# Optimization experiments

Measured on AMD Instinct MI355X. Metric: run time of the kernel, lower is better.

The kernel has to match this reference:

```python
import jax, jax.numpy as jnp
import numpy as np
from jax import lax

# ViT-B/16 geometry hard-coded by the source (197 tokens, 12 heads, head rep of 12)
B, C, IMG, PATCH = 32, 3, 224, 16
E, H, L, P = 768, 12, 12, 16          # embed dim, heads, layers, VPT prompts per layer
NP = (IMG // PATCH) ** 2 + 1          # 197 = cls + 196 patches
S = NP + P                            # 213 tokens after prompt append
HD = E // H
FF = 4 * E
EPS = 1e-6
SCALE = 1.0 / float(HD) ** 0.5


def setup_inputs() -> dict:
    key = jax.random.key(0)
    ks = jax.random.split(key, 12)
    s = 0.02
    return {
        "x": jax.random.normal(ks[0], (B, C, IMG, IMG), jnp.float32),
        "cofficient": jax.random.uniform(ks[1], (L, 1, P), jnp.float32),
        "patch_w": jax.random.normal(ks[2], (E, C, PATCH, PATCH), jnp.float32) * s,
        "patch_b": jnp.zeros((E,), jnp.float32),
        "cls": jax.random.normal(ks[3], (1, 1, E), jnp.float32) * s,
        "pos": jax.random.normal(ks[4], (1, NP, E), jnp.float32) * s,
        "ln_pre_g": jnp.ones((E,), jnp.float32),
        "ln_pre_b": jnp.zeros((E,), jnp.float32),
        "prompts": jax.random.normal(ks[5], (L, P, E), jnp.float32) * s,
        "ln1_g": jnp.ones((L, E), jnp.float32),
        "ln1_b": jnp.zeros((L, E), jnp.float32),
        "qkv_w": jax.random.normal(ks[6], (L, 3 * E, E), jnp.float32) * s,
        "qkv_b": jnp.zeros((L, 3 * E), jnp.float32),
        "proj_w": jax.random.normal(ks[7], (L, E, E), jnp.float32) * s,
        "proj_b": jnp.zeros((L, E), jnp.float32),
        "ln2_g": jnp.ones((L, E), jnp.float32),
        "ln2_b": jnp.zeros((L, E), jnp.float32),
        "fc1_w": jax.random.normal(ks[8], (L, FF, E), jnp.float32) * s,
        "fc1_b": jnp.zeros((L, FF), jnp.float32),
        "fc2_w": jax.random.normal(ks[9], (L, E, FF), jnp.float32) * s,
        "fc2_b": jnp.zeros((L, E), jnp.float32),
        "ln_post_g": jnp.ones((E,), jnp.float32),
        "ln_post_b": jnp.zeros((E,), jnp.float32),
    }


def _ln(x, g, b):
    m = jnp.mean(x, -1, keepdims=True)
    v = jnp.mean(jnp.square(x - m), -1, keepdims=True)
    return (x - m) * lax.rsqrt(v + EPS) * g + b


def reference(x, cofficient, patch_w, patch_b, cls, pos, ln_pre_g, ln_pre_b,
              prompts, ln1_g, ln1_b, qkv_w, qkv_b, proj_w, proj_b,
              ln2_g, ln2_b, fc1_w, fc1_b, fc2_w, fc2_b, ln_post_g, ln_post_b):
    # patch embedding: conv16/16 -> [B, E, 14, 14] -> [B, 196, E]
    h = lax.conv_general_dilated(x, patch_w, (PATCH, PATCH), 'VALID',
                                 dimension_numbers=('NCHW', 'OIHW', 'NCHW'))
    h = h + patch_b[None, :, None, None]
    h = h.reshape(B, E, NP - 1).transpose(0, 2, 1)
    h = jnp.concatenate([jnp.broadcast_to(cls, (B, 1, E)), h], axis=1) + pos
    h = _ln(h, ln_pre_g, ln_pre_b)
    # pad to fixed seq length S; prompt slots are overwritten inside each block
    h = jnp.concatenate([h, jnp.zeros((B, P, E), h.dtype)], axis=1)

    def block(xc, p):
        prompt, coeff, g1, b1, wqkv, bqkv, wo, bo, g2, b2, w1, bb1, w2, bb2 = p
        # deep VPT: replace prompt tokens each layer
        xc = jnp.concatenate([xc[:, :NP], jnp.broadcast_to(prompt[None], (B, P, E))], axis=1)
        hh = _ln(xc, g1, b1)
        qkv = jnp.einsum('bse,fe->bsf', hh, wqkv) + bqkv
        q, k, v = jnp.split(qkv, 3, axis=-1)
        q = q.reshape(B, S, H, HD).transpose(0, 2, 1, 3)
        k = k.reshape(B, S, H, HD).transpose(0, 2, 1, 3)
        v = v.reshape(B, S, H, HD).transpose(0, 2, 1, 3)
        scores = jnp.einsum('bhqd,bhkd->bhqk', q, k) * SCALE   # [B,H,S,S]
        # elementwise coefficient reweighting: ones over 197 base keys, coeff over prompts
        cfull = jnp.concatenate([jnp.ones((NP,), scores.dtype), coeff[0]])
        scores = scores * cfull[None, None, None, :]
        attn = jax.nn.softmax(scores, axis=-1)
        o = jnp.einsum('bhqk,bhkd->bhqd', attn, v).transpose(0, 2, 1, 3).reshape(B, S, E)
        xc = xc + (jnp.einsum('bse,fe->bsf', o, wo) + bo)
        hh = _ln(xc, g2, b2)
        hh = jax.nn.gelu(jnp.einsum('bse,fe->bsf', hh, w1) + bb1, approximate=False)
        xc = xc + (jnp.einsum('bsf,ef->bse', hh, w2) + bb2)
        return xc, None

    params = (prompts, cofficient, ln1_g, ln1_b, qkv_w, qkv_b, proj_w, proj_b,
              ln2_g, ln2_b, fc1_w, fc1_b, fc2_w, fc2_b)
    h, _ = lax.scan(block, h, params)
    return _ln(h[:, 0, :], ln_post_g, ln_post_b)   # [B, E]
```

## Files before the change

kernel.cpp:

```cpp
#include <hip/hip_runtime.h>
#include <hip/hip_bf16.h>

#define B_   32
#define S_   213
#define NP_  197
#define P_   16
#define E_   768
#define H_   12
#define HD_  64
#define FF_  3072
#define L_   12
#define EPS_ 1e-6f
#define SCALE_ 0.125f

typedef __attribute__((ext_vector_type(8))) short short8;
typedef __attribute__((ext_vector_type(4))) float floatx4;

__device__ __forceinline__ ushort f2b(float x) {
  __hip_bfloat16 h = __float2bfloat16(x);
  return __builtin_bit_cast(ushort, h);
}
__device__ __forceinline__ float b2f(ushort u) {
  return __uint_as_float(((unsigned)u) << 16);
}

__device__ __forceinline__ void glds16(const void* g, void* l) {
  __builtin_amdgcn_global_load_lds(
      (const __attribute__((address_space(1))) void*)g,
      (__attribute__((address_space(3))) void*)l, 16, 0, 0);
}

template <int MODE>
__global__ __launch_bounds__(256) void gemm_mfma(
    const ushort* __restrict__ A, const ushort* __restrict__ W,
    const float* __restrict__ bias, float* __restrict__ Cf,
    ushort* __restrict__ Cb, ushort* __restrict__ Vout,
    int M, int N, int K) {
  __shared__ alignas(16) ushort Al[4096];
  __shared__ alignas(16) ushort Wl[4096];
  const int tid = threadIdx.x;
  const int w = tid >> 6, l = tid & 63;
  const int m0 = blockIdx.y * 128, n0 = blockIdx.x * 128;
  const int rw = (w >> 1) * 64, cw = (w & 1) * 64;

  const int mA0 = min(m0 + l, M - 1);
  const int mA1 = min(m0 + 64 + l, M - 1);
  const ushort* Ag0 = A + (size_t)mA0 * K + w * 8;
  const ushort* Ag1 = A + (size_t)mA1 * K + w * 8;
  const ushort* Wg0 = W + (size_t)(n0 + l) * K + w * 8;
  const ushort* Wg1 = W + (size_t)(n0 + 64 + l) * K + w * 8;
  ushort* Ald0 = &Al[w * 1024];
  ushort* Ald1 = &Al[w * 1024 + 512];
  ushort* Wld0 = &Wl[w * 1024];
  ushort* Wld1 = &Wl[w * 1024 + 512];

  floatx4 acc[4][4];
#pragma unroll
  for (int i = 0; i < 4; ++i)
#pragma unroll
    for (int j = 0; j < 4; ++j) acc[i][j] = (floatx4){0.f, 0.f, 0.f, 0.f};

  const int lm = l & 15, lk = l >> 4;

  for (int k0 = 0; k0 < K; k0 += 32) {
    glds16(Ag0 + k0, Ald0);
    glds16(Ag1 + k0, Ald1);
    glds16(Wg0 + k0, Wld0);
    glds16(Wg1 + k0, Wld1);
    __syncthreads();
    short8 af[4], bf[4];
#pragma unroll
    for (int s = 0; s < 4; ++s) {
      af[s] = *(const short8*)&Al[(size_t)(lk * 128 + rw + s * 16 + lm) * 8];
      bf[s] = *(const short8*)&Wl[(size_t)(lk * 128 + cw + s * 16 + lm) * 8];
    }
#pragma unroll
    for (int i = 0; i < 4; ++i)
#pragma unroll
      for (int j = 0; j < 4; ++j)
        acc[i][j] = __builtin_amdgcn_mfma_f32_16x16x32_bf16(
            af[i], bf[j], acc[i][j], 0, 0, 0);
    __syncthreads();
  }

  const int lq = l >> 4;
#pragma unroll
  for (int i = 0; i < 4; ++i) {
    const int row0 = m0 + rw + i * 16 + lq * 4;
#pragma unroll
    for (int j = 0; j < 4; ++j) {
      const int col = n0 + cw + j * 16 + lm;
      const float bc = bias[col];
#pragma unroll
      for (int r = 0; r < 4; ++r) {
        const int row = row0 + r;
        if (row >= M) continue;
        float v = acc[i][j][r] + bc;
        if (MODE == 0) Cb[(size_t)row * N + col] = f2b(v);
        if (MODE == 1) {
          v = 0.5f * v * (1.0f + erff(v * 0.70710678118654752f));
          Cb[(size_t)row * N + col] = f2b(v);
        }
        if (MODE == 2) Cf[(size_t)row * N + col] += v;
        if (MODE == 3) {
          if (col < 1536) {
            Cb[(size_t)row * 1536 + col] = f2b(v);
          } else {
            const int c = col - 1536, hh = c >> 6, dd = c & 63;
            const int bb = row / 213, ss = row % 213;
            Vout[(((size_t)(bb * 12 + hh) * 28 + (ss >> 3)) * 64 + dd) * 8 +
                 (ss & 7)] = f2b(v);
          }
        }
      }
    }
  }
}

__global__ __launch_bounds__(256) void patch_mfma(
    const ushort* __restrict__ xb, const ushort* __restrict__ pwb,
    const float* __restrict__ pb, const float* __restrict__ pos,
    float* __restrict__ xc) {
  __shared__ alignas(16) ushort Al[4096];
  __shared__ alignas(16) ushort Wl[4096];
  const int tid = threadIdx.x;
  const int w = tid >> 6, l = tid & 63;
  const int m0 = blockIdx.y * 128, n0 = blockIdx.x * 128;
  const int rw = (w >> 1) * 64, cw = (w & 1) * 64;

  const int mA0 = m0 + l, mA1 = m0 + 64 + l;
  const int b0 = mA0 / 196, p0 = mA0 % 196, pr0 = p0 / 14, pc0 = p0 % 14;
  const int b1 = mA1 / 196, p1 = mA1 % 196, pr1 = p1 / 14, pc1 = p1 % 14;
  const ushort* Wg0 = pwb + (size_t)(n0 + l) * 768 + w * 8;
  const ushort* Wg1 = pwb + (size_t)(n0 + 64 + l) * 768 + w * 8;
  ushort* Ald0 = &Al[w * 1024];
  ushort* Ald1 = &Al[w * 1024 + 512];
  ushort* Wld0 = &Wl[w * 1024];
  ushort* Wld1 = &Wl[w * 1024 + 512];

  floatx4 acc[4][4];
#pragma unroll
  for (int i = 0; i < 4; ++i)
#pragma unroll
    for (int j = 0; j < 4; ++j) acc[i][j] = (floatx4){0.f, 0.f, 0.f, 0.f};

  const int lm = l & 15, lk = l >> 4;

  for (int k0 = 0; k0 < 768; k0 += 32) {
    const int k = k0 + w * 8;
    const int c = k >> 8, kh = (k >> 4) & 15, kw = k & 15;
    const ushort* a0 =
        xb + ((size_t)(b0 * 3 + c) * 224 + pr0 * 16 + kh) * 224 + pc0 * 16 + kw;
    const ushort* a1 =
        xb + ((size_t)(b1 * 3 + c) * 224 + pr1 * 16 + kh) * 224 + pc1 * 16 + kw;
    glds16(a0, Ald0);
    glds16(a1, Ald1);
    glds16(Wg0 + k0, Wld0);
    glds16(Wg1 + k0, Wld1);
    __syncthreads();
    short8 af[4], bf[4];
#pragma unroll
    for (int s = 0; s < 4; ++s) {
      af[s] = *(const short8*)&Al[(size_t)(lk * 128 + rw + s * 16 + lm) * 8];
      bf[s] = *(const short8*)&Wl[(size_t)(lk * 128 + cw + s * 16 + lm) * 8];
    }
#pragma unroll
    for (int i = 0; i < 4; ++i)
#pragma unroll
      for (int j = 0; j < 4; ++j)
        acc[i][j] = __builtin_amdgcn_mfma_f32_16x16x32_bf16(
            af[i], bf[j], acc[i][j], 0, 0, 0);
    __syncthreads();
  }

  const int lq = l >> 4;
#pragma unroll
  for (int i = 0; i < 4; ++i) {
    const int row0 = m0 + rw + i * 16 + lq * 4;
#pragma unroll
    for (int j = 0; j < 4; ++j) {
      const int col = n0 + cw + j * 16 + lm;
      const float bc = pb[col];
#pragma unroll
      for (int r = 0; r < 4; ++r) {
        const int row = row0 + r;
        const int bb = row / 196, pp = row % 196, t = pp + 1;
        xc[((size_t)bb * S_ + t) * E_ + col] =
            acc[i][j][r] + bc + pos[(size_t)t * E_ + col];
      }
    }
  }
}

__global__ __launch_bounds__(256) void conv_x_kernel(
    const float* __restrict__ x, const float* __restrict__ pw,
    ushort* __restrict__ xb, ushort* __restrict__ pwb) {
  size_t t = (size_t)blockIdx.x * 256 + threadIdx.x;
  const float4* s;
  ushort* d;
  size_t off;
  if (t < 1204224) { s = (const float4*)x;  d = xb;  off = t; }
  else             { s = (const float4*)pw; d = pwb; off = t - 1204224; }
  float4 v = s[off];
  ushort4 r;
  r.x = f2b(v.x); r.y = f2b(v.y); r.z = f2b(v.z); r.w = f2b(v.w);
  *(ushort4*)(d + off * 4) = r;
}

__global__ __launch_bounds__(256) void conv_w_kernel(
    const float* __restrict__ qkvw, const float* __restrict__ projw,
    const float* __restrict__ f1w, const float* __restrict__ f2w,
    ushort* __restrict__ wq, ushort* __restrict__ wp,
    ushort* __restrict__ w1, ushort* __restrict__ w2) {
  size_t t = (size_t)blockIdx.x * 256 + threadIdx.x;
  const float4* s;
  ushort* d;
  size_t off;
  if (t < 442368)       { s = (const float4*)qkvw; d = wq; off = t; }
  else if (t < 589824)  { s = (const float4*)projw; d = wp; off = t - 442368; }
  else if (t < 1179648) { s = (const float4*)f1w;  d = w1; off = t - 589824; }
  else                  { s = (const float4*)f2w;  d = w2; off = t - 1179648; }
  float4 v = s[off];
  ushort4 r;
  r.x = f2b(v.x); r.y = f2b(v.y); r.z = f2b(v.z); r.w = f2b(v.w);
  *(ushort4*)(d + off * 4) = r;
}

__global__ __launch_bounds__(256) void vt_pad_zero(ushort* __restrict__ vt) {
  int idx = blockIdx.x * 256 + threadIdx.x;
  if (idx >= 384 * 64 * 11) return;
  int bh = idx / 704;
  int rem = idx % 704;
  int d = rem / 11, ee = rem % 11;
  int s = 213 + ee;
  vt[(((size_t)bh * 28 + (s >> 3)) * 64 + d) * 8 + (s & 7)] = 0;
}

__global__ __launch_bounds__(256) void init_cls_prompts(
    const float* __restrict__ cls, const float* __restrict__ pos,
    float* __restrict__ xc) {
  int idx = blockIdx.x;
  int b = idx / 17, s = idx % 17;
  int tid = threadIdx.x;
  if (s == 0) {
    for (int e = tid; e < E_; e += 256)
      xc[(size_t)b * S_ * E_ + e] = cls[e] + pos[e];
  } else {
    int t = 196 + s;
    for (int e = tid; e < E_; e += 256)
      xc[((size_t)b * S_ + t) * E_ + e] = 0.f;
  }
}

__device__ inline float2 block_sums(float s, float q) {
  __shared__ float sm[8];
#pragma unroll
  for (int off = 32; off; off >>= 1) {
    s += __shfl_xor(s, off);
    q += __shfl_xor(q, off);
  }
  int lane = threadIdx.x & 63, wid = threadIdx.x >> 6;
  if (lane == 0) { sm[2 * wid] = s; sm[2 * wid + 1] = q; }
  __syncthreads();
  float2 r;
  r.x = sm[0] + sm[2] + sm[4] + sm[6];
  r.y = sm[1] + sm[3] + sm[5] + sm[7];
  return r;
}

__global__ __launch_bounds__(256) void ln_pre_kernel(
    float* __restrict__ xc, const float* __restrict__ g,
    const float* __restrict__ bb) {
  int idx = blockIdx.x;
  int b = idx / NP_, t = idx % NP_;
  float* row = xc + ((size_t)b * S_ + t) * E_;
  int tid = threadIdx.x;
  float v0 = row[tid], v1 = row[tid + 256], v2 = row[tid + 512];
  float2 r = block_sums(v0 + v1 + v2, v0 * v0 + v1 * v1 + v2 * v2);
  float mean = r.x * (1.f / 768.f);
  float var  = r.y * (1.f / 768.f) - mean * mean;
  float rstd = rsqrtf(var + EPS_);
  row[tid]       = (v0 - mean) * rstd * g[tid]       + bb[tid];
  row[tid + 256] = (v1 - mean) * rstd * g[tid + 256] + bb[tid + 256];
  row[tid + 512] = (v2 - mean) * rstd * g[tid + 512] + bb[tid + 512];
}

__global__ __launch_bounds__(256) void ln_block_kernel(
    float* __restrict__ xc, ushort* __restrict__ hh,
    const float* __restrict__ g, const float* __restrict__ bb,
    const float* __restrict__ prompt) {
  int idx = blockIdx.x;
  int b = idx / S_, t = idx % S_;
  float* row = xc + ((size_t)b * S_ + t) * E_;
  ushort* orow = hh + ((size_t)b * S_ + t) * E_;
  int tid = threadIdx.x;
  float v0, v1, v2;
  if (prompt != nullptr && t >= NP_) {
    const float* pr = prompt + (size_t)(t - NP_) * E_;
    v0 = pr[tid]; v1 = pr[tid + 256]; v2 = pr[tid + 512];
    row[tid] = v0; row[tid + 256] = v1; row[tid + 512] = v2;
  } else {
    v0 = row[tid]; v1 = row[tid + 256]; v2 = row[tid + 512];
  }
  float2 r = block_sums(v0 + v1 + v2, v0 * v0 + v1 * v1 + v2 * v2);
  float mean = r.x * (1.f / 768.f);
  float var  = r.y * (1.f / 768.f) - mean * mean;
  float rstd = rsqrtf(var + EPS_);
  orow[tid]       = f2b((v0 - mean) * rstd * g[tid]       + bb[tid]);
  orow[tid + 256] = f2b((v1 - mean) * rstd * g[tid + 256] + bb[tid + 256]);
  orow[tid + 512] = f2b((v2 - mean) * rstd * g[tid + 512] + bb[tid + 512]);
}

__global__ __launch_bounds__(256) void ln_post_kernel(
    const float* __restrict__ xc, const float* __restrict__ g,
    const float* __restrict__ bb, float* __restrict__ out) {
  int b = blockIdx.x;
  const float* row = xc + (size_t)b * S_ * E_;
  int tid = threadIdx.x;
  float v0 = row[tid], v1 = row[tid + 256], v2 = row[tid + 512];
  float2 r = block_sums(v0 + v1 + v2, v0 * v0 + v1 * v1 + v2 * v2);
  float mean = r.x * (1.f / 768.f);
  float var  = r.y * (1.f / 768.f) - mean * mean;
  float rstd = rsqrtf(var + EPS_);
  out[(size_t)b * E_ + tid]       = (v0 - mean) * rstd * g[tid]       + bb[tid];
  out[(size_t)b * E_ + tid + 256] = (v1 - mean) * rstd * g[tid + 256] + bb[tid + 256];
  out[(size_t)b * E_ + tid + 512] = (v2 - mean) * rstd * g[tid + 512] + bb[tid + 512];
}

__global__ __launch_bounds__(256) void attn_mfma(
    const ushort* __restrict__ qk, const ushort* __restrict__ vt,
    const float* __restrict__ coeff, ushort* __restrict__ o) {
  __shared__ alignas(16) ushort Vts[14336];
  __shared__ alignas(16) ushort Pss[4][3808];
  const int bh = blockIdx.x, h = bh % H_, b = bh / H_;
  const int tid = threadIdx.x, w = tid >> 6, lane = tid & 63;
  const int lm = lane & 15, quad = lane >> 4;

  const ushort* vsrc = vt + (size_t)bh * 14336;
#pragma unroll
  for (int i = 0; i < 7; ++i) {
    const int idx = w * 64 + i * 256;
    glds16(vsrc + (size_t)(idx + lane) * 8, &Vts[idx * 8]);
  }
  __syncthreads();

  const ushort* qbase = qk + (size_t)b * S_ * 1536;
  const float f12 = (lm < 5) ? 1.f : coeff[lm - 5];
  const float f13 = (lm < 5) ? coeff[11 + lm] : 0.f;
  ushort* Pw = &Pss[w][0];

  for (int qt = w; qt < 14; qt += 4) {
    const int q0 = qt * 16;
    const int qrow = min(q0 + lm, 212);
    const ushort* qp = qbase + (size_t)qrow * 1536 + h * 64 + quad * 8;
    const short8 a0 = *(const short8*)(qp);
    const short8 a1 = *(const short8*)(qp + 32);

    floatx4 acc[14];
#pragma unroll
    for (int t = 0; t < 14; ++t) {
      const int krow = min(t * 16 + lm, 212);
      const ushort* kp = qbase + (size_t)krow * 1536 + 768 + h * 64 + quad * 8;
      const short8 b0 = *(const short8*)(kp);
      const short8 b1 = *(const short8*)(kp + 32);
      floatx4 c = __builtin_amdgcn_mfma_f32_16x16x32_bf16(
          a0, b0, (floatx4){0.f, 0.f, 0.f, 0.f}, 0, 0, 0);
      acc[t] = __builtin_amdgcn_mfma_f32_16x16x32_bf16(a1, b1, c, 0, 0, 0);
    }

    const int qi = quad * 4;
#pragma unroll
    for (int r = 0; r < 4; ++r) {
      float v[14];
#pragma unroll
      for (int t = 0; t < 14; ++t) {
        float s = acc[t][r] * SCALE_;
        if (t == 12) s *= f12;
        if (t == 13) s = (lm < 5) ? s * f13 : -1e30f;
        v[t] = s;
      }
      float mx = v[0];
#pragma unroll
      for (int t = 1; t < 14; ++t) mx = fmaxf(mx, v[t]);
      mx = fmaxf(mx, __shfl_xor(mx, 1));
      mx = fmaxf(mx, __shfl_xor(mx, 2));
      mx = fmaxf(mx, __shfl_xor(mx, 4));
      mx = fmaxf(mx, __shfl_xor(mx, 8));
      float sum = 0.f;
#pragma unroll
      for (int t = 0; t < 14; ++t) {
        float e = __expf(v[t] - mx);
        v[t] = e;
        sum += e;
      }
      sum += __shfl_xor(sum, 1);
      sum += __shfl_xor(sum, 2);
      sum += __shfl_xor(sum, 4);
      sum += __shfl_xor(sum, 8);
      const float inv = 1.f / sum;
#pragma unroll
      for (int t = 0; t < 14; ++t) {
        const int key = t * 16 + lm;
        Pw[((key >> 3) * 17 + qi + r) * 8 + (key & 7)] = f2b(v[t] * inv);
      }
    }

    short8 pa[7];
#pragma unroll
    for (int c = 0; c < 7; ++c)
      pa[c] = *(const short8*)&Pw[((c * 4 + quad) * 17 + lm) * 8];
#pragma unroll
    for (int nt = 0; nt < 4; ++nt) {
      floatx4 oa = (floatx4){0.f, 0.f, 0.f, 0.f};
#pragma unroll
      for (int c = 0; c < 7; ++c) {
        const short8 vb =
            *(const short8*)&Vts[((c * 4 + quad) * 64 + nt * 16 + lm) * 8];
        oa = __builtin_amdgcn_mfma_f32_16x16x32_bf16(pa[c], vb, oa, 0, 0, 0);
      }
#pragma unroll
      for (int r = 0; r < 4; ++r) {
        const int q = q0 + quad * 4 + r;
        if (q < S_)
          o[((size_t)b * S_ + q) * E_ + h * HD_ + nt * 16 + lm] = f2b(oa[r]);
      }
    }
  }
}

extern "C" void kernel_launch(void* const* d_in, const int* in_sizes, int n_in,
                              void* d_out, int out_size, void* d_ws,
                              size_t ws_size, hipStream_t stream) {
  const float* x         = (const float*)d_in[0];
  const float* cof       = (const float*)d_in[1];
  const float* patch_w   = (const float*)d_in[2];
  const float* patch_b   = (const float*)d_in[3];
  const float* cls       = (const float*)d_in[4];
  const float* pos       = (const float*)d_in[5];
  const float* ln_pre_g  = (const float*)d_in[6];
  const float* ln_pre_b  = (const float*)d_in[7];
  const float* prompts   = (const float*)d_in[8];
  const float* ln1_g     = (const float*)d_in[9];
  const float* ln1_b     = (const float*)d_in[10];
  const float* qkv_w     = (const float*)d_in[11];
  const float* qkv_b     = (const float*)d_in[12];
  const float* proj_w    = (const float*)d_in[13];
  const float* proj_b    = (const float*)d_in[14];
  const float* ln2_g     = (const float*)d_in[15];
  const float* ln2_b     = (const float*)d_in[16];
  const float* fc1_w     = (const float*)d_in[17];
  const float* fc1_b     = (const float*)d_in[18];
  const float* fc2_w     = (const float*)d_in[19];
  const float* fc2_b     = (const float*)d_in[20];
  const float* ln_post_g = (const float*)d_in[21];
  const float* ln_post_b = (const float*)d_in[22];
  float* out = (float*)d_out;

  float* xc  = (float*)d_ws;
  ushort* qk = (ushort*)(xc + 5234688);
  ushort* vt = qk + 10469376;
  ushort* hb = vt + 5505024;
  ushort* fb = hb + 5234688;
  ushort* wq = fb + 20938752;
  ushort* wp = wq + 1769472;
  ushort* w1 = wp + 589824;
  ushort* w2 = w1 + 2359296;
  ushort* xb  = fb;
  ushort* pwb = qk;

  const int M = B_ * S_;
  const dim3 blk(256);

  conv_x_kernel<<<5280, blk, 0, stream>>>(x, patch_w, xb, pwb);
  patch_mfma<<<dim3(6, 49), blk, 0, stream>>>(xb, pwb, patch_b, pos, xc);
  init_cls_prompts<<<B_ * 17, blk, 0, stream>>>(cls, pos, xc);
  ln_pre_kernel<<<B_ * NP_, blk, 0, stream>>>(xc, ln_pre_g, ln_pre_b);
  vt_pad_zero<<<1056, blk, 0, stream>>>(vt);

  for (int l = 0; l < L_; ++l) {
    conv_w_kernel<<<6912, blk, 0, stream>>>(
        qkv_w + (size_t)l * 3 * E_ * E_, proj_w + (size_t)l * E_ * E_,
        fc1_w + (size_t)l * FF_ * E_, fc2_w + (size_t)l * E_ * FF_,
        wq, wp, w1, w2);
    ln_block_kernel<<<B_ * S_, blk, 0, stream>>>(
        xc, hb, ln1_g + l * E_, ln1_b + l * E_,
        prompts + (size_t)l * P_ * E_);
    gemm_mfma<3><<<dim3(18, 54), blk, 0, stream>>>(
        hb, wq, qkv_b + (size_t)l * 3 * E_, nullptr, qk, vt, M, 3 * E_, E_);
    attn_mfma<<<B_ * H_, blk, 0, stream>>>(qk, vt, cof + (size_t)l * P_, hb);
    gemm_mfma<2><<<dim3(6, 54), blk, 0, stream>>>(
        hb, wp, proj_b + (size_t)l * E_, xc, nullptr, nullptr, M, E_, E_);
    ln_block_kernel<<<B_ * S_, blk, 0, stream>>>(
        xc, hb, ln2_g + l * E_, ln2_b + l * E_, nullptr);
    gemm_mfma<1><<<dim3(24, 54), blk, 0, stream>>>(
        hb, w1, fc1_b + (size_t)l * FF_, nullptr, fb, nullptr, M, FF_, E_);
    gemm_mfma<2><<<dim3(6, 54), blk, 0, stream>>>(
        fb, w2, fc2_b + (size_t)l * E_, xc, nullptr, nullptr, M, E_, FF_);
  }

  ln_post_kernel<<<B_, blk, 0, stream>>>(xc, ln_post_g, ln_post_b, out);
}
```

Before: 5.106 ms.

## Triple-buffer GEMM LDS tiles with async prefetch two steps ahead

Replaces the single-buffered global-to-LDS load loop in the MFMA GEMM with a three-stage ring buffer. Loads for iteration it+2 are issued while the current tile is computed, using an explicit vmcnt wait and a single barrier per iteration instead of two syncthreads. This hides global memory latency behind MFMA work. The cost is triple the LDS footprint, which may lower occupancy, plus redundant clamped prefetches of the last tile at the end of the loop.

```diff
diff --git a/kernel.cpp b/kernel.cpp
--- a/kernel.cpp
+++ b/kernel.cpp
@@ -36,8 +36,8 @@
     const float* __restrict__ bias, float* __restrict__ Cf,
     ushort* __restrict__ Cb, ushort* __restrict__ Vout,
     int M, int N, int K) {
-  __shared__ alignas(16) ushort Al[4096];
-  __shared__ alignas(16) ushort Wl[4096];
+  __shared__ alignas(16) ushort Al[3 * 4096];
+  __shared__ alignas(16) ushort Wl[3 * 4096];
   const int tid = threadIdx.x;
   const int w = tid >> 6, l = tid & 63;
   const int m0 = blockIdx.y * 128, n0 = blockIdx.x * 128;
@@ -49,10 +49,17 @@
   const ushort* Ag1 = A + (size_t)mA1 * K + w * 8;
   const ushort* Wg0 = W + (size_t)(n0 + l) * K + w * 8;
   const ushort* Wg1 = W + (size_t)(n0 + 64 + l) * K + w * 8;
-  ushort* Ald0 = &Al[w * 1024];
-  ushort* Ald1 = &Al[w * 1024 + 512];
-  ushort* Wld0 = &Wl[w * 1024];
-  ushort* Wld1 = &Wl[w * 1024 + 512];
+
+  ushort* Ald = &Al[w * 1024];
+  ushort* Wld = &Wl[w * 1024];
+
+#define STAGE_(buf, k0)                          \
+  do {                                           \
+    glds16(Ag0 + (k0), Ald + (buf)*4096);        \
+    glds16(Ag1 + (k0), Ald + (buf)*4096 + 512);  \
+    glds16(Wg0 + (k0), Wld + (buf)*4096);        \
+    glds16(Wg1 + (k0), Wld + (buf)*4096 + 512);  \
+  } while (0)
 
   floatx4 acc[4][4];
 #pragma unroll
@@ -61,18 +68,28 @@
     for (int j = 0; j < 4; ++j) acc[i][j] = (floatx4){0.f, 0.f, 0.f, 0.f};
 
   const int lm = l & 15, lk = l >> 4;
-
-  for (int k0 = 0; k0 < K; k0 += 32) {
-    glds16(Ag0 + k0, Ald0);
-    glds16(Ag1 + k0, Ald1);
-    glds16(Wg0 + k0, Wld0);
-    glds16(Wg1 + k0, Wld1);
-    __syncthreads();
+  const int niter = K >> 5;
+  const int klast = (niter - 1) << 5;
+
+  STAGE_(0, 0);
+  STAGE_(1, 32);
+
+  int buf = 0;
+  for (int it = 0; it < niter; ++it) {
+    asm volatile("s_waitcnt vmcnt(4)" ::: "memory");
+    asm volatile("s_barrier" ::: "memory");
+    {
+      const int kpre = min((it + 2) << 5, klast);
+      const int nbuf = (buf + 2 >= 3) ? buf - 1 : buf + 2;
+      STAGE_(nbuf, kpre);
+    }
+    const ushort* Ab = &Al[buf * 4096];
+    const ushort* Wb = &Wl[buf * 4096];
     short8 af[4], bf[4];
 #pragma unroll
     for (int s = 0; s < 4; ++s) {
-      af[s] = *(const short8*)&Al[(size_t)(lk * 128 + rw + s * 16 + lm) * 8];
-      bf[s] = *(const short8*)&Wl[(size_t)(lk * 128 + cw + s * 16 + lm) * 8];
+      af[s] = *(const short8*)&Ab[(size_t)(lk * 128 + rw + s * 16 + lm) * 8];
+      bf[s] = *(const short8*)&Wb[(size_t)(lk * 128 + cw + s * 16 + lm) * 8];
     }
 #pragma unroll
     for (int i = 0; i < 4; ++i)
@@ -80,8 +97,10 @@
       for (int j = 0; j < 4; ++j)
         acc[i][j] = __builtin_amdgcn_mfma_f32_16x16x32_bf16(
             af[i], bf[j], acc[i][j], 0, 0, 0);
-    __syncthreads();
-  }
+    buf = (buf == 2) ? 0 : buf + 1;
+  }
+  asm volatile("s_waitcnt vmcnt(0)" ::: "memory");
+#undef STAGE_
 
   const int lq = l >> 4;
 #pragma unroll
```

New measurement: 5.369 ms. 5.2% more time.

## Split-K the proj and fc2 GEMMs with atomic accumulation into residual

Applied to the files above, without the earlier changes.

The output-projection and fc2 GEMMs have only 324 blocks (6x54). They now split K across a grid z dimension, 2 ways for proj and 4 ways for fc2, so more workgroups run on the MI355X's compute units. Each split adds its partial result into the fp32 residual with atomicAdd, and only the z=0 slice adds the bias. The costs are more atomic traffic on the residual, a summation order that is no longer deterministic, and more total global writes.

```diff
diff --git a/kernel.cpp b/kernel.cpp
--- a/kernel.cpp
+++ b/kernel.cpp
@@ -35,20 +35,21 @@
     const ushort* __restrict__ A, const ushort* __restrict__ W,
     const float* __restrict__ bias, float* __restrict__ Cf,
     ushort* __restrict__ Cb, ushort* __restrict__ Vout,
-    int M, int N, int K) {
+    int M, int N, int Ks, int Kl) {
   __shared__ alignas(16) ushort Al[4096];
   __shared__ alignas(16) ushort Wl[4096];
   const int tid = threadIdx.x;
   const int w = tid >> 6, l = tid & 63;
   const int m0 = blockIdx.y * 128, n0 = blockIdx.x * 128;
   const int rw = (w >> 1) * 64, cw = (w & 1) * 64;
+  const int koff = blockIdx.z * Kl;
 
   const int mA0 = min(m0 + l, M - 1);
   const int mA1 = min(m0 + 64 + l, M - 1);
-  const ushort* Ag0 = A + (size_t)mA0 * K + w * 8;
-  const ushort* Ag1 = A + (size_t)mA1 * K + w * 8;
-  const ushort* Wg0 = W + (size_t)(n0 + l) * K + w * 8;
-  const ushort* Wg1 = W + (size_t)(n0 + 64 + l) * K + w * 8;
+  const ushort* Ag0 = A + (size_t)mA0 * Ks + koff + w * 8;
+  const ushort* Ag1 = A + (size_t)mA1 * Ks + koff + w * 8;
+  const ushort* Wg0 = W + (size_t)(n0 + l) * Ks + koff + w * 8;
+  const ushort* Wg1 = W + (size_t)(n0 + 64 + l) * Ks + koff + w * 8;
   ushort* Ald0 = &Al[w * 1024];
   ushort* Ald1 = &Al[w * 1024 + 512];
   ushort* Wld0 = &Wl[w * 1024];
@@ -62,7 +63,7 @@
 
   const int lm = l & 15, lk = l >> 4;
 
-  for (int k0 = 0; k0 < K; k0 += 32) {
+  for (int k0 = 0; k0 < Kl; k0 += 32) {
     glds16(Ag0 + k0, Ald0);
     glds16(Ag1 + k0, Ald1);
     glds16(Wg0 + k0, Wld0);
@@ -90,7 +91,7 @@
 #pragma unroll
     for (int j = 0; j < 4; ++j) {
       const int col = n0 + cw + j * 16 + lm;
-      const float bc = bias[col];
+      const float bc = (MODE == 4 && blockIdx.z != 0) ? 0.f : bias[col];
 #pragma unroll
       for (int r = 0; r < 4; ++r) {
         const int row = row0 + r;
@@ -101,7 +102,6 @@
           v = 0.5f * v * (1.0f + erff(v * 0.70710678118654752f));
           Cb[(size_t)row * N + col] = f2b(v);
         }
-        if (MODE == 2) Cf[(size_t)row * N + col] += v;
         if (MODE == 3) {
           if (col < 1536) {
             Cb[(size_t)row * 1536 + col] = f2b(v);
@@ -112,6 +112,7 @@
                  (ss & 7)] = f2b(v);
           }
         }
+        if (MODE == 4) atomicAdd(&Cf[(size_t)row * N + col], v);
       }
     }
   }
@@ -486,16 +487,20 @@
         xc, hb, ln1_g + l * E_, ln1_b + l * E_,
         prompts + (size_t)l * P_ * E_);
     gemm_mfma<3><<<dim3(18, 54), blk, 0, stream>>>(
-        hb, wq, qkv_b + (size_t)l * 3 * E_, nullptr, qk, vt, M, 3 * E_, E_);
+        hb, wq, qkv_b + (size_t)l * 3 * E_, nullptr, qk, vt,
+        M, 3 * E_, E_, E_);
     attn_mfma<<<B_ * H_, blk, 0, stream>>>(qk, vt, cof + (size_t)l * P_, hb);
-    gemm_mfma<2><<<dim3(6, 54), blk, 0, stream>>>(
-        hb, wp, proj_b + (size_t)l * E_, xc, nullptr, nullptr, M, E_, E_);
+    gemm_mfma<4><<<dim3(6, 54, 2), blk, 0, stream>>>(
+        hb, wp, proj_b + (size_t)l * E_, xc, nullptr, nullptr,
+        M, E_, E_, E_ / 2);
     ln_block_kernel<<<B_ * S_, blk, 0, stream>>>(
         xc, hb, ln2_g + l * E_, ln2_b + l * E_, nullptr);
     gemm_mfma<1><<<dim3(24, 54), blk, 0, stream>>>(
-        hb, w1, fc1_b + (size_t)l * FF_, nullptr, fb, nullptr, M, FF_, E_);
-    gemm_mfma<2><<<dim3(6, 54), blk, 0, stream>>>(
-        fb, w2, fc2_b + (size_t)l * E_, xc, nullptr, nullptr, M, E_, FF_);
+        hb, w1, fc1_b + (size_t)l * FF_, nullptr, fb, nullptr,
+        M, FF_, E_, E_);
+    gemm_mfma<4><<<dim3(6, 54, 4), blk, 0, stream>>>(
+        fb, w2, fc2_b + (size_t)l * E_, xc, nullptr, nullptr,
+        M, E_, FF_, FF_ / 4);
   }
 
   ln_post_kernel<<<B_, blk, 0, stream>>>(xc, ln_post_g, ln_post_b, out);
```

Result: slower. 5.414 ms (+6.0%).
